# Performance work log

Measured on AMD Instinct MI355X. Metric: run time of the kernel, lower is better.

Reference implementation:

```python
import math
import jax, jax.numpy as jnp
import numpy as np

NUM_BUCKETS = 32
MAX_DISTANCE = 128
N_HEADS = 16
D_KV = 64


def relative_position_bucket(rel_pos, num_buckets=NUM_BUCKETS, max_distance=MAX_DISTANCE):
    # bidirectional=True path of the original
    n = -rel_pos
    nb = num_buckets // 2
    ret = (n < 0).astype(jnp.int32) * nb
    n = jnp.abs(n)
    max_exact = nb // 2
    is_small = n < max_exact
    val_large = max_exact + (
        jnp.log(n.astype(jnp.float32) / max_exact)
        / math.log(max_distance / max_exact)
        * (nb - max_exact)
    ).astype(jnp.int32)
    val_large = jnp.minimum(val_large, nb - 1)
    return jnp.where(is_small, n, val_large) + ret


def setup_inputs() -> dict:
    key = jax.random.key(0)
    ks = jax.random.split(key, 6)
    B, S, D = 2, 2048, 1024
    inner = N_HEADS * D_KV  # 1024
    sc = 1.0 / math.sqrt(D)
    return {
        "x": jax.random.normal(ks[0], (B, S, D), dtype=jnp.float32),
        "Wq": jax.random.normal(ks[1], (D, inner), dtype=jnp.float32) * sc,
        "Wk": jax.random.normal(ks[2], (D, inner), dtype=jnp.float32) * sc,
        "Wv": jax.random.normal(ks[3], (D, inner), dtype=jnp.float32) * sc,
        "Wo": jax.random.normal(ks[4], (inner, D), dtype=jnp.float32) * sc,
        "rel_table": jax.random.normal(ks[5], (NUM_BUCKETS, N_HEADS), dtype=jnp.float32),
        "attention_mask": jnp.zeros((B, 1, 1, S), dtype=jnp.float32),
    }


def reference(x, Wq, Wk, Wv, Wo, rel_table, attention_mask):
    B, S, D = x.shape
    H, Dk = N_HEADS, D_KV

    q = (x @ Wq).reshape(B, S, H, Dk).transpose(0, 2, 1, 3)  # bhqd
    k = (x @ Wk).reshape(B, S, H, Dk).transpose(0, 2, 1, 3)
    v = (x @ Wv).reshape(B, S, H, Dk).transpose(0, 2, 1, 3)

    # NOTE: T5 attention has no 1/sqrt(d) scaling
    scores = jnp.einsum('bhqd,bhkd->bhqk', q.astype(jnp.float32), k.astype(jnp.float32))

    pos = jnp.arange(S)
    rel_pos = pos[None, :] - pos[:, None]  # [S,S] = k_pos - q_pos
    buckets = relative_position_bucket(rel_pos)
    position_bias = jnp.transpose(rel_table[buckets], (2, 0, 1))  # [H,S,S]

    scores = scores + position_bias[None, ...] + attention_mask
    weights = jax.nn.softmax(scores, axis=-1)
    out = jnp.einsum('bhqk,bhkd->bhqd', weights, v.astype(jnp.float32))
    out = out.transpose(0, 2, 1, 3).reshape(B, S, H * Dk).astype(x.dtype)
    out = out @ Wo
    return (out, position_bias)
```

## Files before the change

### kernel.cpp

```cpp
#include <hip/hip_runtime.h>
#include <hip/hip_bf16.h>
#include <math.h>
#include <stdint.h>

typedef __bf16 bf16_t;
typedef __attribute__((ext_vector_type(8))) __bf16 bf16x8;
typedef __attribute__((ext_vector_type(4))) float f32x4;
typedef unsigned short u16;
typedef unsigned int u32;

#define DEV static __device__ __forceinline__
#define LOG2E 1.4426950408889634f

DEV u16 f2b(float f){ bf16_t h = (bf16_t)f; return __builtin_bit_cast(u16, h); }
DEV float b2f(u16 u){ bf16_t h = __builtin_bit_cast(bf16_t, u); return (float)h; }
DEV f32x4 mfma16(bf16x8 a, bf16x8 b, f32x4 c){
  return __builtin_amdgcn_mfma_f32_16x16x32_bf16(a, b, c, 0, 0, 0);
}

#if __has_builtin(__builtin_amdgcn_exp2f)
DEV float fexp2(float x){ return __builtin_amdgcn_exp2f(x); }
#else
DEV float fexp2(float x){ return exp2f(x); }
#endif

DEV void gld16(const void* g, void* l){
  __builtin_amdgcn_global_load_lds((const __attribute__((address_space(1))) u32*)g,
                                   (__attribute__((address_space(3))) u32*)l, 16, 0, 0);
}

DEV bf16x8 ldsA64(const u16* arr, int row, int ch){
  return *(const bf16x8*)&arr[row*64 + ((ch ^ (row&7))*8)];
}
DEV bf16x8 ldsA32(const u16* arr, int row, int ch){
  return *(const bf16x8*)&arr[row*32 + ((ch ^ ((row>>1)&3))*8)];
}

__global__ __launch_bounds__(256) void k_convert_x(const float* __restrict__ x,
                                                   u16* __restrict__ xh, u16* __restrict__ xl){
  size_t i = ((size_t)blockIdx.x*256 + threadIdx.x)*4;
  float4 v = *(const float4*)(x + i);
  ushort4 hv, lv; float f, hf;
  f=v.x; hv.x=f2b(f); hf=b2f(hv.x); lv.x=f2b(f-hf);
  f=v.y; hv.y=f2b(f); hf=b2f(hv.y); lv.y=f2b(f-hf);
  f=v.z; hv.z=f2b(f); hf=b2f(hv.z); lv.z=f2b(f-hf);
  f=v.w; hv.w=f2b(f); hf=b2f(hv.w); lv.w=f2b(f-hf);
  *(ushort4*)(xh+i) = hv;
  *(ushort4*)(xl+i) = lv;
}

__global__ __launch_bounds__(256) void k_convert_w(const float* __restrict__ Wq, const float* __restrict__ Wk,
                                                   const float* __restrict__ Wv, const float* __restrict__ Wo,
                                                   u16* __restrict__ wth, u16* __restrict__ wtl,
                                                   u16* __restrict__ wot){
  __shared__ float tile[64][65];
  int z = blockIdx.z;
  const float* W = (z==0)?Wq:((z==1)?Wk:((z==2)?Wv:Wo));
  int n0 = blockIdx.x*64, k0 = blockIdx.y*64;
  int t = threadIdx.x;
  int r = t>>6, c = t&63;
  #pragma unroll
  for(int i=0;i<16;i++){
    int row = i*4 + r;
    tile[row][c] = W[(size_t)(k0+row)*1024 + n0 + c];
  }
  __syncthreads();
  #pragma unroll
  for(int i=0;i<16;i++){
    int nrow = i*4 + r;
    float v = tile[c][nrow];
    size_t o = (size_t)(n0+nrow)*1024 + k0 + c;
    u16 hb = f2b(v);
    if(z<3){
      wth[(size_t)z*1048576 + o] = hb;
      wtl[(size_t)z*1048576 + o] = f2b(v - b2f(hb));
    } else {
      wot[o] = hb;
    }
  }
}

__global__ __launch_bounds__(256) void k_bias_table(const float* __restrict__ rel_table,
                                                    const float* __restrict__ mask,
                                                    float* __restrict__ bt, float* __restrict__ bt2,
                                                    float* __restrict__ msk2){
  int gid = blockIdx.x*256 + threadIdx.x;
  if(gid < 4096) msk2[gid] = mask[gid]*LOG2E;
  int h = gid >> 12, idx = gid & 4095;
  float v = 0.f;
  if(idx < 4095){
    int delta = idx - 2047;
    int n = -delta;
    int ret = 0;
    if(n < 0){ ret = 16; n = -n; }
    int bucket;
    if(n < 8) bucket = n + ret;
    else {
      float a = (float)log((double)n * 0.125);
      float rr = (float)((double)a / (double)2.7725887298583984f);
      int vl = 8 + (int)(rr * 8.0f);
      vl = vl > 15 ? 15 : vl;
      bucket = vl + ret;
    }
    v = rel_table[bucket*16 + h];
  }
  bt[gid] = v;
  bt2[gid] = v*LOG2E - 32.0f;
}

__global__ __launch_bounds__(256) void k_write_bias(const float* __restrict__ bt,
                                                    float* __restrict__ out){
  size_t f = ((size_t)blockIdx.x*256 + threadIdx.x)*4;
  int h = (int)(f >> 22);
  int rem = (int)(f & 4194303);
  int q = rem >> 11;
  int k = rem & 2047;
  const float* row = bt + h*4096 + (k - q + 2047);
  float4 v = make_float4(row[0], row[1], row[2], row[3]);
  *(float4*)(out + f) = v;
}

__global__ __launch_bounds__(256) void k_gemm_qkv(const u16* __restrict__ xh, const u16* __restrict__ xl,
                                                  const u16* __restrict__ wth, const u16* __restrict__ wtl,
                                                  u16* __restrict__ qh, u16* __restrict__ ql,
                                                  u16* __restrict__ kh, u16* __restrict__ kl,
                                                  u16* __restrict__ vt){
  __shared__ __align__(16) u16 SM[17408];
  u16* Ah = SM; u16* Al = SM+4096; u16* Bh = SM+8192; u16* Bl = SM+12288;
  int z = blockIdx.z;
  const u16* WH = wth + (size_t)z*1048576;
  const u16* WL = wtl + (size_t)z*1048576;
  int m0 = blockIdx.y*128, n0 = blockIdx.x*128;
  int t = threadIdx.x, w = t>>6, lane = t&63, l16 = lane&15, g = lane>>4;
  const f32x4 fzero = {0.f,0.f,0.f,0.f};
  f32x4 acc[4][4];
  #pragma unroll
  for(int i=0;i<4;i++)
    #pragma unroll
    for(int j=0;j<4;j++) acc[i][j] = fzero;
  int rbase = (w>>1)*64, cbase = (w&1)*64;
  for(int k0=0;k0<1024;k0+=32){
    __syncthreads();
    #pragma unroll
    for(int jj=0;jj<8;jj++){
      int q = w + 4*jj;
      int arr = q>>3, sub = q&7;
      int row = sub*16 + (lane>>2);
      int lch = (lane&3) ^ ((row>>1)&3);
      const u16* src;
      if(arr==0)      src = xh + (size_t)(m0+row)*1024 + k0 + lch*8;
      else if(arr==1) src = xl + (size_t)(m0+row)*1024 + k0 + lch*8;
      else if(arr==2) src = WH + (size_t)(n0+row)*1024 + k0 + lch*8;
      else            src = WL + (size_t)(n0+row)*1024 + k0 + lch*8;
      gld16(src, &SM[q*512]);
    }
    __syncthreads();
    bf16x8 ah[4], am[4];
    #pragma unroll
    for(int i=0;i<4;i++){
      int row = rbase + i*16 + l16;
      ah[i] = ldsA32(Ah, row, g);
      am[i] = ldsA32(Al, row, g);
    }
    #pragma unroll
    for(int j=0;j<4;j++){
      int row = cbase + j*16 + l16;
      bf16x8 bh = ldsA32(Bh, row, g);
      bf16x8 bl = ldsA32(Bl, row, g);
      #pragma unroll
      for(int i=0;i<4;i++){
        acc[i][j] = mfma16(ah[i], bh, acc[i][j]);
        acc[i][j] = mfma16(ah[i], bl, acc[i][j]);
        acc[i][j] = mfma16(am[i], bh, acc[i][j]);
      }
    }
  }
  if(z==2){
    __syncthreads();
    #pragma unroll
    for(int i=0;i<4;i++)
      #pragma unroll
      for(int j=0;j<4;j++)
        #pragma unroll
        for(int r=0;r<4;r++){
          int ml = rbase + i*16 + g*4 + r;
          int nl = cbase + j*16 + l16;
          SM[nl*136 + ml] = f2b(acc[i][j][r]);
        }
    __syncthreads();
    int bb = m0 >> 11;
    #pragma unroll
    for(int kk=0;kk<8;kk++){
      int id = t + 256*kk;
      int row = id>>4, ch = id&15;
      uint4 v = *(const uint4*)&SM[row*136 + ch*8];
      int n = n0 + row;
      size_t dst = ((size_t)(bb*16 + (n>>6))*64 + (n&63))*2048 + (m0&2047) + ch*8;
      *(uint4*)&vt[dst] = v;
    }
  } else {
    #pragma unroll
    for(int i=0;i<4;i++)
      #pragma unroll
      for(int j=0;j<4;j++)
        #pragma unroll
        for(int r=0;r<4;r++){
          int m = m0 + rbase + i*16 + g*4 + r;
          int n = n0 + cbase + j*16 + l16;
          float v = acc[i][j][r];
          if(z==0) v *= LOG2E;
          int b = m >> 11, s = m & 2047;
          int hh = n >> 6, d = n & 63;
          size_t a = ((size_t)(b*16+hh)*2048 + s)*64 + d;
          u16 hb = f2b(v);
          u16 lb = f2b(v - b2f(hb));
          if(z==0){ qh[a]=hb; ql[a]=lb; }
          else    { kh[a]=hb; kl[a]=lb; }
        }
  }
}

__global__ __launch_bounds__(256) void k_attn(const u16* __restrict__ qh, const u16* __restrict__ ql,
                                              const u16* __restrict__ kh, const u16* __restrict__ kl,
                                              const u16* __restrict__ vt, const float* __restrict__ bt2,
                                              const float* __restrict__ msk2, u16* __restrict__ ao){
  __shared__ __align__(16) u16 SM[21504];
  u16* KH = SM; u16* KL = SM+4096; u16* VT = SM+8192;
  int bh = blockIdx.y, b = bh>>4, h = bh&15;
  int q0 = blockIdx.x*128;
  int t = threadIdx.x, w = t>>6, lane = t&63, l16 = lane&15, g = lane>>4;
  size_t base  = (size_t)bh*2048*64;
  size_t vbase = (size_t)bh*64*2048;
  u16* PSw = SM + 12288 + w*2304;
  const float* bt2h = bt2 + h*4096;
  const float* msk2b = msk2 + b*2048;

  bf16x8 qfh[2][2], qfl[2][2];
  #pragma unroll
  for(int i=0;i<2;i++){
    int qr = q0 + w*32 + i*16 + l16;
    size_t a0 = base + (size_t)qr*64 + g*8;
    qfh[i][0] = *(const bf16x8*)&qh[a0];
    qfl[i][0] = *(const bf16x8*)&ql[a0];
    qfh[i][1] = *(const bf16x8*)&qh[a0+32];
    qfl[i][1] = *(const bf16x8*)&ql[a0+32];
  }
  const f32x4 fzero = {0.f,0.f,0.f,0.f};
  f32x4 O[2][4];
  float rs[2][4];
  #pragma unroll
  for(int i=0;i<2;i++){
    #pragma unroll
    for(int jd=0;jd<4;jd++) O[i][jd] = fzero;
    #pragma unroll
    for(int r=0;r<4;r++) rs[i][r] = 0.f;
  }

  for(int k0=0;k0<2048;k0+=64){
    __syncthreads();
    #pragma unroll
    for(int jj=0;jj<6;jj++){
      int q = w + 4*jj;
      int arr = q>>3, sub = q&7;
      int row = sub*8 + (lane>>3);
      int lch = (lane&7) ^ (row&7);
      const u16* src;
      if(arr==0)      src = kh + base + (size_t)(k0+row)*64 + lch*8;
      else if(arr==1) src = kl + base + (size_t)(k0+row)*64 + lch*8;
      else            src = vt + vbase + (size_t)row*2048 + k0 + lch*8;
      gld16(src, &SM[q*512]);
    }
    __syncthreads();
    f32x4 sc[2][4];
    #pragma unroll
    for(int j=0;j<4;j++){
      int krow = j*16 + l16;
      bf16x8 kfh0 = ldsA64(KH, krow, g);
      bf16x8 kfl0 = ldsA64(KL, krow, g);
      bf16x8 kfh1 = ldsA64(KH, krow, 4+g);
      bf16x8 kfl1 = ldsA64(KL, krow, 4+g);
      #pragma unroll
      for(int i=0;i<2;i++){
        f32x4 s = fzero;
        s = mfma16(qfh[i][0], kfh0, s);
        s = mfma16(qfh[i][0], kfl0, s);
        s = mfma16(qfl[i][0], kfh0, s);
        s = mfma16(qfh[i][1], kfh1, s);
        s = mfma16(qfh[i][1], kfl1, s);
        s = mfma16(qfl[i][1], kfh1, s);
        sc[i][j] = s;
      }
    }
    float mkj[4];
    #pragma unroll
    for(int j=0;j<4;j++) mkj[j] = msk2b[k0 + j*16 + l16];
    #pragma unroll
    for(int i=0;i<2;i++){
      const float* bbase = bt2h + (k0 + l16 + 2047 - (q0 + w*32 + i*16 + g*4));
      #pragma unroll
      for(int j=0;j<4;j++){
        const float* bp = bbase + j*16;
        #pragma unroll
        for(int r=0;r<4;r++){
          float tt = sc[i][j][r] + bp[-r] + mkj[j];
          float p = fexp2(tt);
          rs[i][r] += p;
          PSw[(i*16 + g*4 + r)*72 + j*16 + l16] = f2b(p);
        }
      }
    }
    #pragma unroll
    for(int ds=0; ds<2; ds++){
      bf16x8 pa0 = *(const bf16x8*)&PSw[(     l16)*72 + ds*32 + g*8];
      bf16x8 pa1 = *(const bf16x8*)&PSw[(16 + l16)*72 + ds*32 + g*8];
      #pragma unroll
      for(int jd=0;jd<4;jd++){
        bf16x8 vb = ldsA64(VT, jd*16 + l16, ds*4 + g);
        O[0][jd] = mfma16(pa0, vb, O[0][jd]);
        O[1][jd] = mfma16(pa1, vb, O[1][jd]);
      }
    }
  }
  #pragma unroll
  for(int i=0;i<2;i++){
    float inv[4];
    #pragma unroll
    for(int r=0;r<4;r++){
      float v = rs[i][r];
      v += __shfl_xor(v,1,64);
      v += __shfl_xor(v,2,64);
      v += __shfl_xor(v,4,64);
      v += __shfl_xor(v,8,64);
      inv[r] = 1.f/v;
    }
    #pragma unroll
    for(int r=0;r<4;r++){
      int q = q0 + w*32 + i*16 + g*4 + r;
      size_t a = ((size_t)(b*2048 + q))*1024 + h*64;
      #pragma unroll
      for(int jd=0;jd<4;jd++)
        ao[a + jd*16 + l16] = f2b(O[i][jd][r]*inv[r]);
    }
  }
}

__global__ __launch_bounds__(256) void k_gemm_out(const u16* __restrict__ ao, const u16* __restrict__ wot,
                                                  float* __restrict__ out){
  __shared__ __align__(16) u16 SM[8192];
  u16* As = SM; u16* Bs = SM+4096;
  int m0 = blockIdx.y*128, n0 = blockIdx.x*128;
  int t = threadIdx.x, w = t>>6, lane = t&63, l16 = lane&15, g = lane>>4;
  const f32x4 fzero = {0.f,0.f,0.f,0.f};
  f32x4 acc[4][4];
  #pragma unroll
  for(int i=0;i<4;i++)
    #pragma unroll
    for(int j=0;j<4;j++) acc[i][j] = fzero;
  int rbase = (w>>1)*64, cbase = (w&1)*64;
  for(int k0=0;k0<1024;k0+=32){
    __syncthreads();
    #pragma unroll
    for(int jj=0;jj<4;jj++){
      int q = w + 4*jj;
      int arr = q>>3, sub = q&7;
      int row = sub*16 + (lane>>2);
      int lch = (lane&3) ^ ((row>>1)&3);
      const u16* src;
      if(arr==0) src = ao  + (size_t)(m0+row)*1024 + k0 + lch*8;
      else       src = wot + (size_t)(n0+row)*1024 + k0 + lch*8;
      gld16(src, &SM[q*512]);
    }
    __syncthreads();
    bf16x8 af[4];
    #pragma unroll
    for(int i=0;i<4;i++) af[i] = ldsA32(As, rbase + i*16 + l16, g);
    #pragma unroll
    for(int j=0;j<4;j++){
      bf16x8 bfb = ldsA32(Bs, cbase + j*16 + l16, g);
      #pragma unroll
      for(int i=0;i<4;i++)
        acc[i][j] = mfma16(af[i], bfb, acc[i][j]);
    }
  }
  #pragma unroll
  for(int i=0;i<4;i++)
    #pragma unroll
    for(int j=0;j<4;j++)
      #pragma unroll
      for(int r=0;r<4;r++){
        int m = m0 + rbase + i*16 + g*4 + r;
        int n = n0 + cbase + j*16 + l16;
        out[(size_t)m*1024 + n] = acc[i][j][r];
      }
}

extern "C" void kernel_launch(void* const* d_in, const int* in_sizes, int n_in,
                              void* d_out, int out_size, void* d_ws, size_t ws_size,
                              hipStream_t stream) {
  const float* x   = (const float*)d_in[0];
  const float* Wq  = (const float*)d_in[1];
  const float* Wk  = (const float*)d_in[2];
  const float* Wv  = (const float*)d_in[3];
  const float* Wo  = (const float*)d_in[4];
  const float* rel = (const float*)d_in[5];
  const float* msk = (const float*)d_in[6];
  float* out = (float*)d_out;
  float* bias_out = out + (size_t)4194304;
  char* ws = (char*)d_ws;
  u16* xh  = (u16*)(ws + 0);
  u16* xl  = (u16*)(ws + 8388608);
  u16* wth = (u16*)(ws + 16777216);
  u16* wtl = (u16*)(ws + 23068672);
  u16* wot = (u16*)(ws + 29360128);
  u16* qh  = (u16*)(ws + 31457280);
  u16* ql  = (u16*)(ws + 39845888);
  u16* kh  = (u16*)(ws + 48234496);
  u16* kl  = (u16*)(ws + 56623104);
  u16* vt  = (u16*)(ws + 65011712);
  u16* ao  = (u16*)(ws + 73400320);
  float* bt   = (float*)(ws + 81788928);
  float* bt2  = (float*)(ws + 82051072);
  float* msk2 = (float*)(ws + 82313216);

  k_convert_x <<<4096, 256, 0, stream>>>(x, xh, xl);
  k_convert_w <<<dim3(16,16,4), 256, 0, stream>>>(Wq, Wk, Wv, Wo, wth, wtl, wot);
  k_bias_table<<<256, 256, 0, stream>>>(rel, msk, bt, bt2, msk2);
  k_write_bias<<<65536, 256, 0, stream>>>(bt, bias_out);
  k_gemm_qkv  <<<dim3(8,32,3), 256, 0, stream>>>(xh, xl, wth, wtl, qh, ql, kh, kl, vt);
  k_attn      <<<dim3(16,32), 256, 0, stream>>>(qh, ql, kh, kl, vt, bt2, msk2, ao);
  k_gemm_out  <<<dim3(8,32), 256, 0, stream>>>(ao, wot, out);
}
```

Before: 540.2 us.

## Drop low-order bf16 terms for K and V, prefill scores with bias

The V projection now runs as a single-pass bf16 GEMM that skips loading the low-order x and W halves. K is stored only as a high bf16 part, so the QK^T product drops from 6 to 4 MFMAs per tile and the attention kernel no longer loads a KL tile. Position bias and mask are loaded before the barrier and used as the MFMA accumulator's initial value. This cuts MFMA work, LDS traffic and global loads, at the cost of lower precision in the scores and V, which may affect accuracy against the fp32 reference.

```diff
diff --git a/kernel.cpp b/kernel.cpp
--- a/kernel.cpp
+++ b/kernel.cpp
@@ -123,8 +123,7 @@
 __global__ __launch_bounds__(256) void k_gemm_qkv(const u16* __restrict__ xh, const u16* __restrict__ xl,
                                                   const u16* __restrict__ wth, const u16* __restrict__ wtl,
                                                   u16* __restrict__ qh, u16* __restrict__ ql,
-                                                  u16* __restrict__ kh, u16* __restrict__ kl,
-                                                  u16* __restrict__ vt){
+                                                  u16* __restrict__ kh, u16* __restrict__ vt){
   __shared__ __align__(16) u16 SM[17408];
   u16* Ah = SM; u16* Al = SM+4096; u16* Bh = SM+8192; u16* Bl = SM+12288;
   int z = blockIdx.z;
@@ -145,6 +144,7 @@
     for(int jj=0;jj<8;jj++){
       int q = w + 4*jj;
       int arr = q>>3, sub = q&7;
+      if(z==2 && (arr&1)) continue;
       int row = sub*16 + (lane>>2);
       int lch = (lane&3) ^ ((row>>1)&3);
       const u16* src;
@@ -155,23 +155,36 @@
       gld16(src, &SM[q*512]);
     }
     __syncthreads();
-    bf16x8 ah[4], am[4];
-    #pragma unroll
-    for(int i=0;i<4;i++){
-      int row = rbase + i*16 + l16;
-      ah[i] = ldsA32(Ah, row, g);
-      am[i] = ldsA32(Al, row, g);
-    }
-    #pragma unroll
-    for(int j=0;j<4;j++){
-      int row = cbase + j*16 + l16;
-      bf16x8 bh = ldsA32(Bh, row, g);
-      bf16x8 bl = ldsA32(Bl, row, g);
+    if(z==2){
+      bf16x8 ah[4];
+      #pragma unroll
+      for(int i=0;i<4;i++) ah[i] = ldsA32(Ah, rbase + i*16 + l16, g);
+      #pragma unroll
+      for(int j=0;j<4;j++){
+        bf16x8 bh = ldsA32(Bh, cbase + j*16 + l16, g);
+        #pragma unroll
+        for(int i=0;i<4;i++)
+          acc[i][j] = mfma16(ah[i], bh, acc[i][j]);
+      }
+    } else {
+      bf16x8 ah[4], am[4];
       #pragma unroll
       for(int i=0;i<4;i++){
-        acc[i][j] = mfma16(ah[i], bh, acc[i][j]);
-        acc[i][j] = mfma16(ah[i], bl, acc[i][j]);
-        acc[i][j] = mfma16(am[i], bh, acc[i][j]);
+        int row = rbase + i*16 + l16;
+        ah[i] = ldsA32(Ah, row, g);
+        am[i] = ldsA32(Al, row, g);
+      }
+      #pragma unroll
+      for(int j=0;j<4;j++){
+        int row = cbase + j*16 + l16;
+        bf16x8 bh = ldsA32(Bh, row, g);
+        bf16x8 bl = ldsA32(Bl, row, g);
+        #pragma unroll
+        for(int i=0;i<4;i++){
+          acc[i][j] = mfma16(ah[i], bh, acc[i][j]);
+          acc[i][j] = mfma16(ah[i], bl, acc[i][j]);
+          acc[i][j] = mfma16(am[i], bh, acc[i][j]);
+        }
       }
     }
   }
@@ -213,25 +226,24 @@
           int hh = n >> 6, d = n & 63;
           size_t a = ((size_t)(b*16+hh)*2048 + s)*64 + d;
           u16 hb = f2b(v);
-          u16 lb = f2b(v - b2f(hb));
-          if(z==0){ qh[a]=hb; ql[a]=lb; }
-          else    { kh[a]=hb; kl[a]=lb; }
+          if(z==0){ qh[a]=hb; ql[a]=f2b(v - b2f(hb)); }
+          else    { kh[a]=hb; }
         }
   }
 }
 
 __global__ __launch_bounds__(256) void k_attn(const u16* __restrict__ qh, const u16* __restrict__ ql,
-                                              const u16* __restrict__ kh, const u16* __restrict__ kl,
+                                              const u16* __restrict__ kh,
                                               const u16* __restrict__ vt, const float* __restrict__ bt2,
                                               const float* __restrict__ msk2, u16* __restrict__ ao){
-  __shared__ __align__(16) u16 SM[21504];
-  u16* KH = SM; u16* KL = SM+4096; u16* VT = SM+8192;
+  __shared__ __align__(16) u16 SM[17408];
+  u16* KH = SM; u16* VT = SM+4096;
   int bh = blockIdx.y, b = bh>>4, h = bh&15;
   int q0 = blockIdx.x*128;
   int t = threadIdx.x, w = t>>6, lane = t&63, l16 = lane&15, g = lane>>4;
   size_t base  = (size_t)bh*2048*64;
   size_t vbase = (size_t)bh*64*2048;
-  u16* PSw = SM + 12288 + w*2304;
+  u16* PSw = SM + 8192 + w*2304;
   const float* bt2h = bt2 + h*4096;
   const float* msk2b = msk2 + b*2048;
 
@@ -245,13 +257,12 @@
     qfh[i][1] = *(const bf16x8*)&qh[a0+32];
     qfl[i][1] = *(const bf16x8*)&ql[a0+32];
   }
-  const f32x4 fzero = {0.f,0.f,0.f,0.f};
   f32x4 O[2][4];
   float rs[2][4];
   #pragma unroll
   for(int i=0;i<2;i++){
     #pragma unroll
-    for(int jd=0;jd<4;jd++) O[i][jd] = fzero;
+    for(int jd=0;jd<4;jd++) O[i][jd] = {0.f,0.f,0.f,0.f};
     #pragma unroll
     for(int r=0;r<4;r++) rs[i][r] = 0.f;
   }
@@ -259,51 +270,53 @@
   for(int k0=0;k0<2048;k0+=64){
     __syncthreads();
     #pragma unroll
-    for(int jj=0;jj<6;jj++){
+    for(int jj=0;jj<4;jj++){
       int q = w + 4*jj;
       int arr = q>>3, sub = q&7;
       int row = sub*8 + (lane>>3);
       int lch = (lane&7) ^ (row&7);
       const u16* src;
-      if(arr==0)      src = kh + base + (size_t)(k0+row)*64 + lch*8;
-      else if(arr==1) src = kl + base + (size_t)(k0+row)*64 + lch*8;
-      else            src = vt + vbase + (size_t)row*2048 + k0 + lch*8;
+      if(arr==0) src = kh + base + (size_t)(k0+row)*64 + lch*8;
+      else       src = vt + vbase + (size_t)row*2048 + k0 + lch*8;
       gld16(src, &SM[q*512]);
     }
-    __syncthreads();
+    float mkj[4];
+    #pragma unroll
+    for(int j=0;j<4;j++) mkj[j] = msk2b[k0 + j*16 + l16];
     f32x4 sc[2][4];
+    #pragma unroll
+    for(int i=0;i<2;i++){
+      const float* bb = bt2h + (k0 + l16 + 2047 - (q0 + w*32 + i*16 + g*4));
+      #pragma unroll
+      for(int j=0;j<4;j++){
+        #pragma unroll
+        for(int r=0;r<4;r++)
+          sc[i][j][r] = bb[j*16 - r] + mkj[j];
+      }
+    }
+    __syncthreads();
     #pragma unroll
     for(int j=0;j<4;j++){
       int krow = j*16 + l16;
       bf16x8 kfh0 = ldsA64(KH, krow, g);
-      bf16x8 kfl0 = ldsA64(KL, krow, g);
       bf16x8 kfh1 = ldsA64(KH, krow, 4+g);
-      bf16x8 kfl1 = ldsA64(KL, krow, 4+g);
       #pragma unroll
       for(int i=0;i<2;i++){
-        f32x4 s = fzero;
+        f32x4 s = sc[i][j];
         s = mfma16(qfh[i][0], kfh0, s);
-        s = mfma16(qfh[i][0], kfl0, s);
         s = mfma16(qfl[i][0], kfh0, s);
         s = mfma16(qfh[i][1], kfh1, s);
-        s = mfma16(qfh[i][1], kfl1, s);
         s = mfma16(qfl[i][1], kfh1, s);
         sc[i][j] = s;
       }
     }
-    float mkj[4];
-    #pragma unroll
-    for(int j=0;j<4;j++) mkj[j] = msk2b[k0 + j*16 + l16];
     #pragma unroll
     for(int i=0;i<2;i++){
-      const float* bbase = bt2h + (k0 + l16 + 2047 - (q0 + w*32 + i*16 + g*4));
       #pragma unroll
       for(int j=0;j<4;j++){
-        const float* bp = bbase + j*16;
         #pragma unroll
         for(int r=0;r<4;r++){
-          float tt = sc[i][j][r] + bp[-r] + mkj[j];
-          float p = fexp2(tt);
+          float p = fexp2(sc[i][j][r]);
           rs[i][r] += p;
           PSw[(i*16 + g*4 + r)*72 + j*16 + l16] = f2b(p);
         }
@@ -350,12 +363,11 @@
   u16* As = SM; u16* Bs = SM+4096;
   int m0 = blockIdx.y*128, n0 = blockIdx.x*128;
   int t = threadIdx.x, w = t>>6, lane = t&63, l16 = lane&15, g = lane>>4;
-  const f32x4 fzero = {0.f,0.f,0.f,0.f};
   f32x4 acc[4][4];
   #pragma unroll
   for(int i=0;i<4;i++)
     #pragma unroll
-    for(int j=0;j<4;j++) acc[i][j] = fzero;
+    for(int j=0;j<4;j++) acc[i][j] = {0.f,0.f,0.f,0.f};
   int rbase = (w>>1)*64, cbase = (w&1)*64;
   for(int k0=0;k0<1024;k0+=32){
     __syncthreads();
@@ -415,7 +427,6 @@
   u16* qh  = (u16*)(ws + 31457280);
   u16* ql  = (u16*)(ws + 39845888);
   u16* kh  = (u16*)(ws + 48234496);
-  u16* kl  = (u16*)(ws + 56623104);
   u16* vt  = (u16*)(ws + 65011712);
   u16* ao  = (u16*)(ws + 73400320);
   float* bt   = (float*)(ws + 81788928);
@@ -426,7 +437,7 @@
   k_convert_w <<<dim3(16,16,4), 256, 0, stream>>>(Wq, Wk, Wv, Wo, wth, wtl, wot);
   k_bias_table<<<256, 256, 0, stream>>>(rel, msk, bt, bt2, msk2);
   k_write_bias<<<65536, 256, 0, stream>>>(bt, bias_out);
-  k_gemm_qkv  <<<dim3(8,32,3), 256, 0, stream>>>(xh, xl, wth, wtl, qh, ql, kh, kl, vt);
-  k_attn      <<<dim3(16,32), 256, 0, stream>>>(qh, ql, kh, kl, vt, bt2, msk2, ao);
+  k_gemm_qkv  <<<dim3(8,32,3), 256, 0, stream>>>(xh, xl, wth, wtl, qh, ql, kh, vt);
+  k_attn      <<<dim3(16,32), 256, 0, stream>>>(qh, ql, kh, vt, bt2, msk2, ao);
   k_gemm_out  <<<dim3(8,32), 256, 0, stream>>>(ao, wot, out);
 }
```

Result: no change. 532.2 us (-1.5%).
